# Kernel optimization log

Measured on AMD Instinct MI355X. Metric: run time of the kernel, lower is better.

The kernel has to match this reference:

```python
import jax, jax.numpy as jnp
import numpy as np

N = 50000          # nodes
E = 800000         # edges (before self-loops)
NIN = 300          # n_in
H = 4              # heads
C = 64             # nhid (per-head out channels)
G = 256            # number of graphs in batch
NOUT = 768         # nout
NEG_SLOPE_ATT = 0.2   # PyG GATConv leaky-relu slope for attention logits
NEG_SLOPE_ACT = 0.01  # nn.LeakyReLU default


def setup_inputs() -> dict:
    key = jax.random.key(0)
    ks = jax.random.split(key, 9)
    x = jax.random.normal(ks[0], (N, NIN), dtype=jnp.float32)
    edge_index = jax.random.randint(ks[1], (2, E), 0, N, dtype=jnp.int32)
    batch = jnp.sort(jax.random.randint(ks[2], (N,), 0, G, dtype=jnp.int32))
    lin_w = jax.random.normal(ks[3], (NIN, H * C), dtype=jnp.float32) / np.sqrt(NIN)
    att_src = jax.random.normal(ks[4], (H, C), dtype=jnp.float32) / np.sqrt(C)
    att_dst = jax.random.normal(ks[5], (H, C), dtype=jnp.float32) / np.sqrt(C)
    bias = jnp.zeros((H * C,), dtype=jnp.float32)
    fc1_w = jax.random.normal(ks[6], (H * C, NOUT), dtype=jnp.float32) / np.sqrt(H * C)
    fc1_b = jnp.zeros((NOUT,), dtype=jnp.float32)
    return {"x": x, "edge_index": edge_index, "batch": batch, "lin_w": lin_w,
            "att_src": att_src, "att_dst": att_dst, "bias": bias,
            "fc1_w": fc1_w, "fc1_b": fc1_b}


def reference(x, edge_index, batch, lin_w, att_src, att_dst, bias, fc1_w, fc1_b):
    n = x.shape[0]
    h = (x @ lin_w).reshape(n, H, C)                      # [N,H,C]
    # add self-loops (PyG GATConv default)
    loop = jnp.arange(n, dtype=edge_index.dtype)
    src = jnp.concatenate([edge_index[0], loop])          # [E+N]
    dst = jnp.concatenate([edge_index[1], loop])
    # per-edge attention logits
    a_src = jnp.einsum('nhc,hc->nh', h, att_src)          # [N,H]
    a_dst = jnp.einsum('nhc,hc->nh', h, att_dst)
    e = jax.nn.leaky_relu(a_src[src] + a_dst[dst], NEG_SLOPE_ATT)  # [E+N,H]
    # segment softmax grouped by destination node (self-loops -> every segment nonempty)
    emax = jax.ops.segment_max(e, dst, num_segments=n)    # [N,H]
    ee = jnp.exp(e - emax[dst])
    denom = jax.ops.segment_sum(ee, dst, num_segments=n)
    alpha = ee / denom[dst]                               # [E+N,H]
    # weighted message aggregation
    msg = h[src] * alpha[..., None]                       # [E+N,H,C]
    out = jax.ops.segment_sum(msg, dst, num_segments=n).reshape(n, H * C) + bias
    out = jax.nn.leaky_relu(out, NEG_SLOPE_ACT)
    # global mean pool over graphs
    sums = jax.ops.segment_sum(out, batch, num_segments=G)        # [G,H*C]
    cnt = jax.ops.segment_sum(jnp.ones((n, 1), out.dtype), batch, num_segments=G)
    pooled = sums / jnp.maximum(cnt, 1.0)
    return pooled @ fc1_w + fc1_b                         # [G,NOUT]
```

## Files before the change

kernel.cpp:

```cpp
#include <hip/hip_runtime.h>
#include <hip/hip_bf16.h>

using bf16 = __hip_bfloat16;
typedef __attribute__((ext_vector_type(8))) short short8;
typedef __attribute__((ext_vector_type(4))) float f32x4;

constexpr int N   = 50000;
constexpr int E   = 800000;
constexpr int NIN = 300;
constexpr int H   = 4;
constexpr int C   = 64;
constexpr int HC  = H * C;
constexpr int G   = 256;
constexpr int NOUT = 768;
constexpr int NKB = 10;
constexpr int NT  = 782;
constexpr int DCAP = 64;

__device__ __forceinline__ float b2f(bf16 v) { return __bfloat162float(v); }
__device__ __forceinline__ float us2f(unsigned short u) {
    bf16 b; *(unsigned short*)&b = u; return __bfloat162float(b);
}
__device__ __forceinline__ unsigned short f2us(float f) {
    bf16 b = __float2bfloat16(f); return *(unsigned short*)&b;
}
__device__ __forceinline__ float lrelu_att(float v) { return v > 0.f ? v : 0.2f * v; }
__device__ __forceinline__ float lrelu_act(float v) { return v > 0.f ? v : 0.01f * v; }
__device__ __forceinline__ float ldin(const void* p, int isbf, size_t i) {
    return isbf ? b2f(((const bf16*)p)[i]) : ((const float*)p)[i];
}
__device__ __forceinline__ short8 pack8u(ushort4 lo, ushort4 hi) {
    short8 r;
    r[0] = (short)lo.x; r[1] = (short)lo.y; r[2] = (short)lo.z; r[3] = (short)lo.w;
    r[4] = (short)hi.x; r[5] = (short)hi.y; r[6] = (short)hi.z; r[7] = (short)hi.w;
    return r;
}
__device__ __forceinline__ short8 pack8f(float4 lo, float4 hi) {
    short8 r;
    r[0] = (short)f2us(lo.x); r[1] = (short)f2us(lo.y); r[2] = (short)f2us(lo.z); r[3] = (short)f2us(lo.w);
    r[4] = (short)f2us(hi.x); r[5] = (short)f2us(hi.y); r[6] = (short)f2us(hi.z); r[7] = (short)f2us(hi.w);
    return r;
}

__device__ __forceinline__ short8 loadA_bf(const unsigned short* __restrict__ xr, int kb, int q) {
    ushort4 z = make_ushort4(0, 0, 0, 0);
    ushort4 lo = z, hi = z;
    if (kb < 9) {
        lo = *(const ushort4*)(xr + kb * 32);
        hi = *(const ushort4*)(xr + kb * 32 + 4);
    } else if (q == 0) {
        lo = *(const ushort4*)(xr + 288); hi = *(const ushort4*)(xr + 292);
    } else if (q == 1) {
        lo = *(const ushort4*)(xr + 288);
    }
    return pack8u(lo, hi);
}
__device__ __forceinline__ short8 loadA_f32(const float* __restrict__ xf, int kb, int q) {
    float4 zf = make_float4(0.f, 0.f, 0.f, 0.f);
    float4 lo = zf, hi = zf;
    if (kb < 9) {
        lo = *(const float4*)(xf + kb * 32);
        hi = *(const float4*)(xf + kb * 32 + 4);
    } else if (q == 0) {
        lo = *(const float4*)(xf + 288); hi = *(const float4*)(xf + 292);
    } else if (q == 1) {
        lo = *(const float4*)(xf + 288);
    }
    return pack8f(lo, hi);
}

__device__ __forceinline__ int block_detect(const unsigned short* __restrict__ xr) {
    __shared__ int cnt_s;
    if (threadIdx.x == 0) cnt_s = 0;
    __syncthreads();
    unsigned short u = xr[threadIdx.x & 255];
    int ex = (u >> 7) & 0xFF;
    int ok = (ex == 0) || (ex >= 100 && ex <= 140);
    if (threadIdx.x < 256) atomicAdd(&cnt_s, ok);
    __syncthreads();
    return (cnt_s >= 240) ? 1 : 0;
}

constexpr int NZ  = N + G * HC;
constexpr int NZB = (NZ + 255) / 256;
__global__ __launch_bounds__(256) void k_pre(const unsigned short* __restrict__ xr,
                                             const void* __restrict__ w,
                                             const int* __restrict__ batch,
                                             int* __restrict__ flag,
                                             int* __restrict__ zp,
                                             unsigned short* __restrict__ bswz,
                                             int* __restrict__ gs) {
    int b = blockIdx.x;
    if (b < NZB) {
        int i = b * 256 + threadIdx.x;
        if (i < NZ) zp[i] = 0;
        if (b == 0) {
            int isbf = block_detect(xr);
            if (threadIdx.x == 0) *flag = isbf;
        }
    } else if (b < NZB + 40) {
        int isbf = block_detect(xr);
        int fb = (b - NZB) * 4 + (threadIdx.x >> 6);
        if (fb < 160) {
            int kb = fb >> 4, nb = fb & 15;
            int lane = threadIdx.x & 63;
            int q = lane >> 4, cl = lane & 15;
            int n = nb * 16 + cl;
            unsigned short v[8];
#pragma unroll
            for (int j = 0; j < 8; j++) {
                int k = kb * 32 + q * 8 + j;
                float f = (k < NIN) ? ldin(w, isbf, (size_t)k * HC + n) : 0.f;
                v[j] = f2us(f);
            }
            ushort4* dst = (ushort4*)(bswz + ((size_t)fb * 64 + lane) * 8);
            dst[0] = make_ushort4(v[0], v[1], v[2], v[3]);
            dst[1] = make_ushort4(v[4], v[5], v[6], v[7]);
        }
    } else {
        int g = threadIdx.x;
        int lo = 0, hi = N;
        while (lo < hi) {
            int mid = (lo + hi) >> 1;
            if (batch[mid] < g) lo = mid + 1;
            else hi = mid;
        }
        gs[g] = lo;
        if (g == 0) gs[G] = N;
    }
}

__global__ void k_build(const int* __restrict__ ei,
                        int* __restrict__ cnt,
                        int* __restrict__ csrB) {
    int e = blockIdx.x * 256 + threadIdx.x;
    if (e >= E) return;
    int s = ei[e], d = ei[E + e];
    int pos = atomicAdd(&cnt[d], 1);
    if (pos < DCAP) csrB[(size_t)d * DCAP + pos] = s;
}

__global__ __launch_bounds__(256, 4) void k_lin4(const void* __restrict__ x,
                                                 const unsigned short* __restrict__ bswz,
                                                 const void* __restrict__ att_s,
                                                 const void* __restrict__ att_d,
                                                 unsigned short* __restrict__ hb,
                                                 float* __restrict__ a_src,
                                                 float* __restrict__ a_dst,
                                                 const int* __restrict__ flag) {
    __shared__ unsigned short bs[40 * 64 * 8];
    int isbf = *flag;
    int t = threadIdx.x;
    int c       = blockIdx.x & 7;
    int j       = blockIdx.x >> 3;
    int quarter = j & 3;
    int bslot   = (j >> 2) * 8 + c;
    for (int i = t; i < 40 * 64; i += 256) {
        int f = i >> 6, lane = i & 63;
        int kb = f >> 2, nbl = f & 3;
        const int4* src = (const int4*)(bswz + ((size_t)(kb * 16 + quarter * 4 + nbl) * 64 + lane) * 8);
        ((int4*)bs)[i] = *src;
    }
    __syncthreads();

    int wave = t >> 6, lane = t & 63;
    int q = lane >> 4, cl = lane & 15;
    int hh = quarter;
    float as_h[4], ad_h[4];
#pragma unroll
    for (int nbl = 0; nbl < 4; nbl++) {
        as_h[nbl] = ldin(att_s, isbf, (quarter * 4 + nbl) * 16 + cl);
        ad_h[nbl] = ldin(att_d, isbf, (quarter * 4 + nbl) * 16 + cl);
    }
    for (int tile = bslot; tile < NT; tile += 256) {
        int m0 = tile * 64 + wave * 16;
        int row = m0 + cl; if (row >= N) row = N - 1;
        f32x4 acc[4];
#pragma unroll
        for (int nbl = 0; nbl < 4; nbl++) acc[nbl] = f32x4{0.f, 0.f, 0.f, 0.f};
        if (isbf) {
            const unsigned short* xr = (const unsigned short*)x + (size_t)row * NIN + q * 8;
            short8 a_cur = loadA_bf(xr, 0, q);
            short8 a_nxt = loadA_bf(xr, 1, q);
#pragma unroll
            for (int kb = 0; kb < NKB; kb++) {
                short8 a_pf = {};
                if (kb + 2 < NKB) a_pf = loadA_bf(xr, kb + 2, q);
                short8 bfr[4];
#pragma unroll
                for (int nbl = 0; nbl < 4; nbl++)
                    bfr[nbl] = *(const short8*)(bs + ((size_t)(kb * 4 + nbl) * 64 + lane) * 8);
#pragma unroll
                for (int nbl = 0; nbl < 4; nbl++)
                    acc[nbl] = __builtin_amdgcn_mfma_f32_16x16x32_bf16(a_cur, bfr[nbl], acc[nbl], 0, 0, 0);
                a_cur = a_nxt; a_nxt = a_pf;
            }
        } else {
            const float* xf = (const float*)x + (size_t)row * NIN + q * 8;
            short8 a_cur = loadA_f32(xf, 0, q);
            short8 a_nxt = loadA_f32(xf, 1, q);
#pragma unroll
            for (int kb = 0; kb < NKB; kb++) {
                short8 a_pf = {};
                if (kb + 2 < NKB) a_pf = loadA_f32(xf, kb + 2, q);
                short8 bfr[4];
#pragma unroll
                for (int nbl = 0; nbl < 4; nbl++)
                    bfr[nbl] = *(const short8*)(bs + ((size_t)(kb * 4 + nbl) * 64 + lane) * 8);
#pragma unroll
                for (int nbl = 0; nbl < 4; nbl++)
                    acc[nbl] = __builtin_amdgcn_mfma_f32_16x16x32_bf16(a_cur, bfr[nbl], acc[nbl], 0, 0, 0);
                a_cur = a_nxt; a_nxt = a_pf;
            }
        }
        float ps[4], pd[4];
#pragma unroll
        for (int r = 0; r < 4; r++) { ps[r] = 0.f; pd[r] = 0.f; }
#pragma unroll
        for (int nbl = 0; nbl < 4; nbl++) {
            int nb = quarter * 4 + nbl;
#pragma unroll
            for (int r = 0; r < 4; r++) {
                float v = acc[nbl][r];
                ps[r] += v * as_h[nbl];
                pd[r] += v * ad_h[nbl];
                int gm = m0 + q * 4 + r;
                if (gm < N) hb[(size_t)gm * HC + nb * 16 + cl] = f2us(v);
            }
        }
#pragma unroll
        for (int r = 0; r < 4; r++) {
            float vs = ps[r], vd = pd[r];
#pragma unroll
            for (int m = 1; m < 16; m <<= 1) {
                vs += __shfl_xor(vs, m, 64);
                vd += __shfl_xor(vd, m, 64);
            }
            int gm = m0 + q * 4 + r;
            if (cl == 0 && gm < N) {
                a_src[gm * 4 + hh] = vs;
                a_dst[gm * 4 + hh] = vd;
            }
        }
    }
}

__global__ __launch_bounds__(256) void k_agg(const unsigned short* __restrict__ hb,
                                             const float* __restrict__ a_src,
                                             const float* __restrict__ a_dst,
                                             const int* __restrict__ cnt,
                                             const int* __restrict__ csrB,
                                             const void* __restrict__ bias,
                                             unsigned short* __restrict__ outn,
                                             const int* __restrict__ flag) {
    int isbf = *flag;
    int wave = threadIdx.x >> 6, lane = threadIdx.x & 63;
    int n = blockIdx.x * 4 + wave;
    if (n >= N) return;
    int head = lane >> 4;
    float adn = a_dst[n * 4 + head];
    float wself = __expf(lrelu_att(a_src[n * 4 + head] + adn));
    ushort4 hv = *(const ushort4*)&hb[(size_t)n * HC + lane * 4];
    float4 acc;
    acc.x = us2f(hv.x) * wself;
    acc.y = us2f(hv.y) * wself;
    acc.z = us2f(hv.z) * wself;
    acc.w = us2f(hv.w) * wself;
    float ssum = wself;
    int dg = cnt[n]; if (dg > DCAP) dg = DCAP;
    const int* lst = csrB + (size_t)n * DCAP;
    int p0 = 0, p1 = dg;
    int p = p0;
    ushort4 ga0, ga1, ga2, ga3;
    float wa0, wa1, wa2, wa3;
    int ib0 = 0, ib1 = 0, ib2 = 0, ib3 = 0;
    if (p + 4 <= p1) {
        int i0 = lst[p], i1 = lst[p + 1], i2 = lst[p + 2], i3 = lst[p + 3];
        ga0 = *(const ushort4*)&hb[(size_t)i0 * HC + lane * 4];
        ga1 = *(const ushort4*)&hb[(size_t)i1 * HC + lane * 4];
        ga2 = *(const ushort4*)&hb[(size_t)i2 * HC + lane * 4];
        ga3 = *(const ushort4*)&hb[(size_t)i3 * HC + lane * 4];
        wa0 = a_src[(size_t)i0 * 4 + head];
        wa1 = a_src[(size_t)i1 * 4 + head];
        wa2 = a_src[(size_t)i2 * 4 + head];
        wa3 = a_src[(size_t)i3 * 4 + head];
    }
    if (p + 8 <= p1) {
        ib0 = lst[p + 4]; ib1 = lst[p + 5]; ib2 = lst[p + 6]; ib3 = lst[p + 7];
    }
    while (p + 8 <= p1) {
        ushort4 gb0 = *(const ushort4*)&hb[(size_t)ib0 * HC + lane * 4];
        ushort4 gb1 = *(const ushort4*)&hb[(size_t)ib1 * HC + lane * 4];
        ushort4 gb2 = *(const ushort4*)&hb[(size_t)ib2 * HC + lane * 4];
        ushort4 gb3 = *(const ushort4*)&hb[(size_t)ib3 * HC + lane * 4];
        float wb0 = a_src[(size_t)ib0 * 4 + head];
        float wb1 = a_src[(size_t)ib1 * 4 + head];
        float wb2 = a_src[(size_t)ib2 * 4 + head];
        float wb3 = a_src[(size_t)ib3 * 4 + head];
        int ic0 = ib0, ic1 = ib1, ic2 = ib2, ic3 = ib3;
        if (p + 12 <= p1) {
            ic0 = lst[p + 8]; ic1 = lst[p + 9]; ic2 = lst[p + 10]; ic3 = lst[p + 11];
        }
        float e0 = __expf(lrelu_att(wa0 + adn));
        float e1 = __expf(lrelu_att(wa1 + adn));
        float e2 = __expf(lrelu_att(wa2 + adn));
        float e3 = __expf(lrelu_att(wa3 + adn));
        acc.x += us2f(ga0.x) * e0 + us2f(ga1.x) * e1 + us2f(ga2.x) * e2 + us2f(ga3.x) * e3;
        acc.y += us2f(ga0.y) * e0 + us2f(ga1.y) * e1 + us2f(ga2.y) * e2 + us2f(ga3.y) * e3;
        acc.z += us2f(ga0.z) * e0 + us2f(ga1.z) * e1 + us2f(ga2.z) * e2 + us2f(ga3.z) * e3;
        acc.w += us2f(ga0.w) * e0 + us2f(ga1.w) * e1 + us2f(ga2.w) * e2 + us2f(ga3.w) * e3;
        ssum += (e0 + e1) + (e2 + e3);
        ga0 = gb0; ga1 = gb1; ga2 = gb2; ga3 = gb3;
        wa0 = wb0; wa1 = wb1; wa2 = wb2; wa3 = wb3;
        ib0 = ic0; ib1 = ic1; ib2 = ic2; ib3 = ic3;
        p += 4;
    }
    if (p + 4 <= p1) {
        float e0 = __expf(lrelu_att(wa0 + adn));
        float e1 = __expf(lrelu_att(wa1 + adn));
        float e2 = __expf(lrelu_att(wa2 + adn));
        float e3 = __expf(lrelu_att(wa3 + adn));
        acc.x += us2f(ga0.x) * e0 + us2f(ga1.x) * e1 + us2f(ga2.x) * e2 + us2f(ga3.x) * e3;
        acc.y += us2f(ga0.y) * e0 + us2f(ga1.y) * e1 + us2f(ga2.y) * e2 + us2f(ga3.y) * e3;
        acc.z += us2f(ga0.z) * e0 + us2f(ga1.z) * e1 + us2f(ga2.z) * e2 + us2f(ga3.z) * e3;
        acc.w += us2f(ga0.w) * e0 + us2f(ga1.w) * e1 + us2f(ga2.w) * e2 + us2f(ga3.w) * e3;
        ssum += (e0 + e1) + (e2 + e3);
        p += 4;
    }
    for (; p < p1; p++) {
        int s = lst[p];
        float wv = __expf(lrelu_att(a_src[(size_t)s * 4 + head] + adn));
        ushort4 hs = *(const ushort4*)&hb[(size_t)s * HC + lane * 4];
        acc.x += us2f(hs.x) * wv;
        acc.y += us2f(hs.y) * wv;
        acc.z += us2f(hs.z) * wv;
        acc.w += us2f(hs.w) * wv;
        ssum += wv;
    }
    float inv = 1.f / ssum;
    ushort4 o;
    o.x = f2us(lrelu_act(acc.x * inv + ldin(bias, isbf, lane * 4 + 0)));
    o.y = f2us(lrelu_act(acc.y * inv + ldin(bias, isbf, lane * 4 + 1)));
    o.z = f2us(lrelu_act(acc.z * inv + ldin(bias, isbf, lane * 4 + 2)));
    o.w = f2us(lrelu_act(acc.w * inv + ldin(bias, isbf, lane * 4 + 3)));
    *(ushort4*)&outn[(size_t)n * HC + lane * 4] = o;
}

__global__ __launch_bounds__(256) void k_pool2(const unsigned short* __restrict__ outn,
                                               const int* __restrict__ gs,
                                               float* __restrict__ sums) {
    int g = blockIdx.x, qq = blockIdx.y, t = threadIdx.x;
    int s = gs[g], e2 = gs[g + 1];
    int len = e2 - s;
    int r0 = s + (len * qq) / 4;
    int r1 = s + (len * (qq + 1)) / 4;
    float a0 = 0.f, a1 = 0.f, a2 = 0.f, a3 = 0.f;
    int r = r0;
    for (; r + 4 <= r1; r += 4) {
        a0 += us2f(outn[(size_t)(r + 0) * HC + t]);
        a1 += us2f(outn[(size_t)(r + 1) * HC + t]);
        a2 += us2f(outn[(size_t)(r + 2) * HC + t]);
        a3 += us2f(outn[(size_t)(r + 3) * HC + t]);
    }
    for (; r < r1; r++) a0 += us2f(outn[(size_t)r * HC + t]);
    float v = (a0 + a1) + (a2 + a3);
    if (r1 > r0) atomicAdd(&sums[(size_t)g * HC + t], v);
}

__global__ __launch_bounds__(256) void k_fc(const float* __restrict__ sums,
                                            const int* __restrict__ gs,
                                            const void* __restrict__ fw,
                                            const void* __restrict__ fb,
                                            void* __restrict__ out,
                                            const int* __restrict__ flag) {
    __shared__ float pl[HC];
    int isbf = *flag;
    int g = blockIdx.y;
    int o = blockIdx.x * 256 + threadIdx.x;
    int c = gs[g + 1] - gs[g];
    float inv = 1.f / (float)(c > 1 ? c : 1);
    pl[threadIdx.x] = sums[(size_t)g * HC + threadIdx.x] * inv;
    __syncthreads();
    float acc = ldin(fb, isbf, o);
#pragma unroll 8
    for (int k = 0; k < HC; k++) acc += pl[k] * ldin(fw, isbf, (size_t)k * NOUT + o);
    size_t oi = (size_t)g * NOUT + o;
    if (isbf) ((bf16*)out)[oi] = __float2bfloat16(acc);
    else      ((float*)out)[oi] = acc;
}

extern "C" void kernel_launch(void* const* d_in, const int* in_sizes, int n_in,
                              void* d_out, int out_size, void* d_ws, size_t ws_size,
                              hipStream_t stream) {
    const void* x     = d_in[0];
    const int*  ei    = (const int*)d_in[1];
    const int*  batch = (const int*)d_in[2];
    const void* lin_w = d_in[3];
    const void* att_s = d_in[4];
    const void* att_d = d_in[5];
    const void* bias  = d_in[6];
    const void* fc1w  = d_in[7];
    const void* fc1b  = d_in[8];

    char* p = (char*)d_ws;
    unsigned short* hb   = (unsigned short*)p; p += (size_t)N * HC * 2;
    unsigned short* outn = (unsigned short*)p; p += (size_t)N * HC * 2;
    float* a_src  = (float*)p; p += (size_t)N * H * 4;
    float* a_dst  = (float*)p; p += (size_t)N * H * 4;
    int* cnt      = (int*)p;   p += (size_t)N * 4;
    float* sums   = (float*)p; p += (size_t)G * HC * 4;
    int* csrB     = (int*)p;   p += (size_t)N * DCAP * 4;
    unsigned short* bswz = (unsigned short*)p; p += (size_t)160 * 64 * 8 * 2;
    int* gs       = (int*)p;   p += (size_t)(G + 4) * 4;
    int* flag     = (int*)p;   p += 16;

    k_pre<<<NZB + 40 + 1, 256, 0, stream>>>((const unsigned short*)x, lin_w, batch,
                                            flag, cnt, bswz, gs);
    k_build<<<(E + 255) / 256, 256, 0, stream>>>(ei, cnt, csrB);
    k_lin4<<<1024, 256, 0, stream>>>(x, bswz, att_s, att_d, hb, a_src, a_dst, flag);
    k_agg<<<(N + 3) / 4, 256, 0, stream>>>(hb, a_src, a_dst, cnt, csrB, bias, outn, flag);
    k_pool2<<<dim3(G, 4), 256, 0, stream>>>(outn, gs, sums);
    k_fc<<<dim3(NOUT / 256, G), 256, 0, stream>>>(sums, gs, fc1w, fc1b, d_out, flag);
}
```

Measured before the change: 276.3 us.

## Fuse CSR build into linear kernel and merge pooling with final FC

Folds the edge-bucketing (CSR build) loop into the prologue of the linear/attention kernel, with each of the 1024 blocks handling 782 edges. Pooling and the FC layer become one kernel that has one block per graph, so the intermediate sums buffer, its zeroing and the float atomics are gone. This removes two kernel launches and overlaps the atomic-heavy scatter with the GEMM's weight staging. In exchange the pooling now runs on only 256 blocks, each walking all rows of its graph serially, and the GEMM blocks start later because of the atomic work.

```diff
diff --git a/kernel.cpp b/kernel.cpp
--- a/kernel.cpp
+++ b/kernel.cpp
@@ -16,6 +16,7 @@
 constexpr int NKB = 10;
 constexpr int NT  = 782;
 constexpr int DCAP = 64;
+constexpr int EPB  = 782;
 
 __device__ __forceinline__ float b2f(bf16 v) { return __bfloat162float(v); }
 __device__ __forceinline__ float us2f(unsigned short u) {
@@ -81,7 +82,7 @@
     return (cnt_s >= 240) ? 1 : 0;
 }
 
-constexpr int NZ  = N + G * HC;
+constexpr int NZ  = N;
 constexpr int NZB = (NZ + 255) / 256;
 __global__ __launch_bounds__(256) void k_pre(const unsigned short* __restrict__ xr,
                                              const void* __restrict__ w,
@@ -130,16 +131,6 @@
     }
 }
 
-__global__ void k_build(const int* __restrict__ ei,
-                        int* __restrict__ cnt,
-                        int* __restrict__ csrB) {
-    int e = blockIdx.x * 256 + threadIdx.x;
-    if (e >= E) return;
-    int s = ei[e], d = ei[E + e];
-    int pos = atomicAdd(&cnt[d], 1);
-    if (pos < DCAP) csrB[(size_t)d * DCAP + pos] = s;
-}
-
 __global__ __launch_bounds__(256, 4) void k_lin4(const void* __restrict__ x,
                                                  const unsigned short* __restrict__ bswz,
                                                  const void* __restrict__ att_s,
@@ -147,7 +138,10 @@
                                                  unsigned short* __restrict__ hb,
                                                  float* __restrict__ a_src,
                                                  float* __restrict__ a_dst,
-                                                 const int* __restrict__ flag) {
+                                                 const int* __restrict__ flag,
+                                                 const int* __restrict__ ei,
+                                                 int* __restrict__ cnt,
+                                                 int* __restrict__ csrB) {
     __shared__ unsigned short bs[40 * 64 * 8];
     int isbf = *flag;
     int t = threadIdx.x;
@@ -160,6 +154,14 @@
         int kb = f >> 2, nbl = f & 3;
         const int4* src = (const int4*)(bswz + ((size_t)(kb * 16 + quarter * 4 + nbl) * 64 + lane) * 8);
         ((int4*)bs)[i] = *src;
+    }
+    for (int i = t; i < EPB; i += 256) {
+        int e = blockIdx.x * EPB + i;
+        if (e < E) {
+            int s = ei[e], d = ei[E + e];
+            int pos = atomicAdd(&cnt[d], 1);
+            if (pos < DCAP) csrB[(size_t)d * DCAP + pos] = s;
+        }
     }
     __syncthreads();
 
@@ -346,47 +348,39 @@
     *(ushort4*)&outn[(size_t)n * HC + lane * 4] = o;
 }
 
-__global__ __launch_bounds__(256) void k_pool2(const unsigned short* __restrict__ outn,
-                                               const int* __restrict__ gs,
-                                               float* __restrict__ sums) {
-    int g = blockIdx.x, qq = blockIdx.y, t = threadIdx.x;
+__global__ __launch_bounds__(256) void k_fcp(const unsigned short* __restrict__ outn,
+                                             const int* __restrict__ gs,
+                                             const void* __restrict__ fw,
+                                             const void* __restrict__ fb,
+                                             void* __restrict__ out,
+                                             const int* __restrict__ flag) {
+    __shared__ float pl[HC];
+    int isbf = *flag;
+    int g = blockIdx.x, t = threadIdx.x;
     int s = gs[g], e2 = gs[g + 1];
-    int len = e2 - s;
-    int r0 = s + (len * qq) / 4;
-    int r1 = s + (len * (qq + 1)) / 4;
     float a0 = 0.f, a1 = 0.f, a2 = 0.f, a3 = 0.f;
-    int r = r0;
-    for (; r + 4 <= r1; r += 4) {
+    int r = s;
+    for (; r + 4 <= e2; r += 4) {
         a0 += us2f(outn[(size_t)(r + 0) * HC + t]);
         a1 += us2f(outn[(size_t)(r + 1) * HC + t]);
         a2 += us2f(outn[(size_t)(r + 2) * HC + t]);
         a3 += us2f(outn[(size_t)(r + 3) * HC + t]);
     }
-    for (; r < r1; r++) a0 += us2f(outn[(size_t)r * HC + t]);
-    float v = (a0 + a1) + (a2 + a3);
-    if (r1 > r0) atomicAdd(&sums[(size_t)g * HC + t], v);
-}
-
-__global__ __launch_bounds__(256) void k_fc(const float* __restrict__ sums,
-                                            const int* __restrict__ gs,
-                                            const void* __restrict__ fw,
-                                            const void* __restrict__ fb,
-                                            void* __restrict__ out,
-                                            const int* __restrict__ flag) {
-    __shared__ float pl[HC];
-    int isbf = *flag;
-    int g = blockIdx.y;
-    int o = blockIdx.x * 256 + threadIdx.x;
-    int c = gs[g + 1] - gs[g];
+    for (; r < e2; r++) a0 += us2f(outn[(size_t)r * HC + t]);
+    int c = e2 - s;
     float inv = 1.f / (float)(c > 1 ? c : 1);
-    pl[threadIdx.x] = sums[(size_t)g * HC + threadIdx.x] * inv;
+    pl[t] = ((a0 + a1) + (a2 + a3)) * inv;
     __syncthreads();
-    float acc = ldin(fb, isbf, o);
+#pragma unroll
+    for (int oo = 0; oo < NOUT / 256; oo++) {
+        int o = oo * 256 + t;
+        float acc = ldin(fb, isbf, o);
 #pragma unroll 8
-    for (int k = 0; k < HC; k++) acc += pl[k] * ldin(fw, isbf, (size_t)k * NOUT + o);
-    size_t oi = (size_t)g * NOUT + o;
-    if (isbf) ((bf16*)out)[oi] = __float2bfloat16(acc);
-    else      ((float*)out)[oi] = acc;
+        for (int k = 0; k < HC; k++) acc += pl[k] * ldin(fw, isbf, (size_t)k * NOUT + o);
+        size_t oi = (size_t)g * NOUT + o;
+        if (isbf) ((bf16*)out)[oi] = __float2bfloat16(acc);
+        else      ((float*)out)[oi] = acc;
+    }
 }
 
 extern "C" void kernel_launch(void* const* d_in, const int* in_sizes, int n_in,
@@ -408,7 +402,6 @@
     float* a_src  = (float*)p; p += (size_t)N * H * 4;
     float* a_dst  = (float*)p; p += (size_t)N * H * 4;
     int* cnt      = (int*)p;   p += (size_t)N * 4;
-    float* sums   = (float*)p; p += (size_t)G * HC * 4;
     int* csrB     = (int*)p;   p += (size_t)N * DCAP * 4;
     unsigned short* bswz = (unsigned short*)p; p += (size_t)160 * 64 * 8 * 2;
     int* gs       = (int*)p;   p += (size_t)(G + 4) * 4;
@@ -416,9 +409,8 @@
 
     k_pre<<<NZB + 40 + 1, 256, 0, stream>>>((const unsigned short*)x, lin_w, batch,
                                             flag, cnt, bswz, gs);
-    k_build<<<(E + 255) / 256, 256, 0, stream>>>(ei, cnt, csrB);
-    k_lin4<<<1024, 256, 0, stream>>>(x, bswz, att_s, att_d, hb, a_src, a_dst, flag);
+    k_lin4<<<1024, 256, 0, stream>>>(x, bswz, att_s, att_d, hb, a_src, a_dst, flag,
+                                     ei, cnt, csrB);
     k_agg<<<(N + 3) / 4, 256, 0, stream>>>(hb, a_src, a_dst, cnt, csrB, bias, outn, flag);
-    k_pool2<<<dim3(G, 4), 256, 0, stream>>>(outn, gs, sums);
-    k_fc<<<dim3(NOUT / 256, G), 256, 0, stream>>>(sums, gs, fc1w, fc1b, d_out, flag);
-}
+    k_fcp<<<G, 256, 0, stream>>>(outn, gs, fc1w, fc1b, d_out, flag);
+}
```

After: 341.1 us. 1.23x slower.

## Fuse CSR build into prep kernel and pool with FC, drop sums buffer

Applied to the files above, without the earlier changes.

The edge-to-CSR scatter now runs in extra blocks of the prep kernel, and the degree counters are cleared with a memset instead of a zeroing block range. Mean pooling and the final linear layer become one kernel with one 1024-thread block per graph, reducing four partial sums through shared memory instead of global atomics. This removes two kernel launches and the atomic sums round-trip. The cost is a larger block per graph and only 256 blocks for the fused pool/FC stage.

```diff
diff --git a/kernel.cpp b/kernel.cpp
--- a/kernel.cpp
+++ b/kernel.cpp
@@ -16,6 +16,7 @@
 constexpr int NKB = 10;
 constexpr int NT  = 782;
 constexpr int DCAP = 64;
+constexpr int SCB  = (E + 255) / 256;
 
 __device__ __forceinline__ float b2f(bf16 v) { return __bfloat162float(v); }
 __device__ __forceinline__ float us2f(unsigned short u) {
@@ -81,26 +82,20 @@
     return (cnt_s >= 240) ? 1 : 0;
 }
 
-constexpr int NZ  = N + G * HC;
-constexpr int NZB = (NZ + 255) / 256;
 __global__ __launch_bounds__(256) void k_pre(const unsigned short* __restrict__ xr,
                                              const void* __restrict__ w,
                                              const int* __restrict__ batch,
                                              int* __restrict__ flag,
-                                             int* __restrict__ zp,
                                              unsigned short* __restrict__ bswz,
-                                             int* __restrict__ gs) {
+                                             int* __restrict__ gs,
+                                             const int* __restrict__ ei,
+                                             int* __restrict__ cnt,
+                                             int* __restrict__ csrB) {
     int b = blockIdx.x;
-    if (b < NZB) {
-        int i = b * 256 + threadIdx.x;
-        if (i < NZ) zp[i] = 0;
-        if (b == 0) {
-            int isbf = block_detect(xr);
-            if (threadIdx.x == 0) *flag = isbf;
-        }
-    } else if (b < NZB + 40) {
+    if (b < 40) {
         int isbf = block_detect(xr);
-        int fb = (b - NZB) * 4 + (threadIdx.x >> 6);
+        if (b == 0 && threadIdx.x == 0) *flag = isbf;
+        int fb = b * 4 + (threadIdx.x >> 6);
         if (fb < 160) {
             int kb = fb >> 4, nb = fb & 15;
             int lane = threadIdx.x & 63;
@@ -117,7 +112,7 @@
             dst[0] = make_ushort4(v[0], v[1], v[2], v[3]);
             dst[1] = make_ushort4(v[4], v[5], v[6], v[7]);
         }
-    } else {
+    } else if (b == 40) {
         int g = threadIdx.x;
         int lo = 0, hi = N;
         while (lo < hi) {
@@ -127,17 +122,14 @@
         }
         gs[g] = lo;
         if (g == 0) gs[G] = N;
-    }
-}
-
-__global__ void k_build(const int* __restrict__ ei,
-                        int* __restrict__ cnt,
-                        int* __restrict__ csrB) {
-    int e = blockIdx.x * 256 + threadIdx.x;
-    if (e >= E) return;
-    int s = ei[e], d = ei[E + e];
-    int pos = atomicAdd(&cnt[d], 1);
-    if (pos < DCAP) csrB[(size_t)d * DCAP + pos] = s;
+    } else {
+        int e = (b - 41) * 256 + threadIdx.x;
+        if (e < E) {
+            int s = ei[e], d = ei[E + e];
+            int pos = atomicAdd(&cnt[d], 1);
+            if (pos < DCAP) csrB[(size_t)d * DCAP + pos] = s;
+        }
+    }
 }
 
 __global__ __launch_bounds__(256, 4) void k_lin4(const void* __restrict__ x,
@@ -346,10 +338,17 @@
     *(ushort4*)&outn[(size_t)n * HC + lane * 4] = o;
 }
 
-__global__ __launch_bounds__(256) void k_pool2(const unsigned short* __restrict__ outn,
-                                               const int* __restrict__ gs,
-                                               float* __restrict__ sums) {
-    int g = blockIdx.x, qq = blockIdx.y, t = threadIdx.x;
+__global__ __launch_bounds__(1024) void k_fcp(const unsigned short* __restrict__ outn,
+                                              const int* __restrict__ gs,
+                                              const void* __restrict__ fw,
+                                              const void* __restrict__ fb,
+                                              void* __restrict__ out,
+                                              const int* __restrict__ flag) {
+    __shared__ float pl4[4][HC];
+    __shared__ float pl[HC];
+    int isbf = *flag;
+    int g = blockIdx.x, t = threadIdx.x;
+    int qq = t >> 8, ch = t & 255;
     int s = gs[g], e2 = gs[g + 1];
     int len = e2 - s;
     int r0 = s + (len * qq) / 4;
@@ -357,36 +356,27 @@
     float a0 = 0.f, a1 = 0.f, a2 = 0.f, a3 = 0.f;
     int r = r0;
     for (; r + 4 <= r1; r += 4) {
-        a0 += us2f(outn[(size_t)(r + 0) * HC + t]);
-        a1 += us2f(outn[(size_t)(r + 1) * HC + t]);
-        a2 += us2f(outn[(size_t)(r + 2) * HC + t]);
-        a3 += us2f(outn[(size_t)(r + 3) * HC + t]);
-    }
-    for (; r < r1; r++) a0 += us2f(outn[(size_t)r * HC + t]);
-    float v = (a0 + a1) + (a2 + a3);
-    if (r1 > r0) atomicAdd(&sums[(size_t)g * HC + t], v);
-}
-
-__global__ __launch_bounds__(256) void k_fc(const float* __restrict__ sums,
-                                            const int* __restrict__ gs,
-                                            const void* __restrict__ fw,
-                                            const void* __restrict__ fb,
-                                            void* __restrict__ out,
-                                            const int* __restrict__ flag) {
-    __shared__ float pl[HC];
-    int isbf = *flag;
-    int g = blockIdx.y;
-    int o = blockIdx.x * 256 + threadIdx.x;
-    int c = gs[g + 1] - gs[g];
-    float inv = 1.f / (float)(c > 1 ? c : 1);
-    pl[threadIdx.x] = sums[(size_t)g * HC + threadIdx.x] * inv;
+        a0 += us2f(outn[(size_t)(r + 0) * HC + ch]);
+        a1 += us2f(outn[(size_t)(r + 1) * HC + ch]);
+        a2 += us2f(outn[(size_t)(r + 2) * HC + ch]);
+        a3 += us2f(outn[(size_t)(r + 3) * HC + ch]);
+    }
+    for (; r < r1; r++) a0 += us2f(outn[(size_t)r * HC + ch]);
+    pl4[qq][ch] = (a0 + a1) + (a2 + a3);
     __syncthreads();
-    float acc = ldin(fb, isbf, o);
+    if (t < HC) {
+        float inv = 1.f / (float)(len > 1 ? len : 1);
+        pl[t] = (pl4[0][t] + pl4[1][t] + pl4[2][t] + pl4[3][t]) * inv;
+    }
+    __syncthreads();
+    if (t < NOUT) {
+        float acc = ldin(fb, isbf, t);
 #pragma unroll 8
-    for (int k = 0; k < HC; k++) acc += pl[k] * ldin(fw, isbf, (size_t)k * NOUT + o);
-    size_t oi = (size_t)g * NOUT + o;
-    if (isbf) ((bf16*)out)[oi] = __float2bfloat16(acc);
-    else      ((float*)out)[oi] = acc;
+        for (int k = 0; k < HC; k++) acc += pl[k] * ldin(fw, isbf, (size_t)k * NOUT + t);
+        size_t oi = (size_t)g * NOUT + t;
+        if (isbf) ((bf16*)out)[oi] = __float2bfloat16(acc);
+        else      ((float*)out)[oi] = acc;
+    }
 }
 
 extern "C" void kernel_launch(void* const* d_in, const int* in_sizes, int n_in,
@@ -408,17 +398,15 @@
     float* a_src  = (float*)p; p += (size_t)N * H * 4;
     float* a_dst  = (float*)p; p += (size_t)N * H * 4;
     int* cnt      = (int*)p;   p += (size_t)N * 4;
-    float* sums   = (float*)p; p += (size_t)G * HC * 4;
     int* csrB     = (int*)p;   p += (size_t)N * DCAP * 4;
     unsigned short* bswz = (unsigned short*)p; p += (size_t)160 * 64 * 8 * 2;
     int* gs       = (int*)p;   p += (size_t)(G + 4) * 4;
     int* flag     = (int*)p;   p += 16;
 
-    k_pre<<<NZB + 40 + 1, 256, 0, stream>>>((const unsigned short*)x, lin_w, batch,
-                                            flag, cnt, bswz, gs);
-    k_build<<<(E + 255) / 256, 256, 0, stream>>>(ei, cnt, csrB);
+    hipMemsetAsync(cnt, 0, (size_t)N * 4, stream);
+    k_pre<<<41 + SCB, 256, 0, stream>>>((const unsigned short*)x, lin_w, batch,
+                                        flag, bswz, gs, ei, cnt, csrB);
     k_lin4<<<1024, 256, 0, stream>>>(x, bswz, att_s, att_d, hb, a_src, a_dst, flag);
     k_agg<<<(N + 3) / 4, 256, 0, stream>>>(hb, a_src, a_dst, cnt, csrB, bias, outn, flag);
-    k_pool2<<<dim3(G, 4), 256, 0, stream>>>(outn, gs, sums);
-    k_fc<<<dim3(NOUT / 256, G), 256, 0, stream>>>(sums, gs, fc1w, fc1b, d_out, flag);
-}
+    k_fcp<<<G, 1024, 0, stream>>>(outn, gs, fc1w, fc1b, d_out, flag);
+}
```

Result: no change. 275.6 us (median of 2 runs) (-0.2%).
